# Optimization experiments

Measured on AMD Instinct MI355X. Metric: run time of the kernel, lower is better.

Reference implementation:

```python
import jax, jax.numpy as jnp
import numpy as np

# YOLOLayer config (matches init_kwargs)
ANCHORS = [(0.1, 0.13), (0.3, 0.35), (0.6, 0.55)]  # (w, h) as fraction of image
NUM_CLASSES = 80
STRIDE = 8
NA = len(ANCHORS)


def setup_inputs() -> dict:
    key = jax.random.key(0)
    B, C, G = 16, NA * (NUM_CLASSES + 5), 64
    x = jax.random.normal(key, (B, C, G, G), dtype=jnp.float32)
    return {"x": x}


def reference(x):
    B = x.shape[0]
    g0, g1 = x.shape[2], x.shape[3]
    nC = NUM_CLASSES
    # [B, nA, g0, g1, 5+nC]
    pred = x.reshape(B, NA, nC + 5, g0, g1).transpose(0, 1, 3, 4, 2)
    sx = jax.nn.sigmoid(pred[..., 0])
    sy = jax.nn.sigmoid(pred[..., 1])
    w = pred[..., 2]
    h = pred[..., 3]
    pred_conf = jax.nn.sigmoid(pred[..., 4])
    pred_cls = jax.nn.sigmoid(pred[..., 5:])

    # grid offsets: grid_x varies along last dim, grid_y along dim -2 (torch semantics)
    grid_x = jnp.arange(g1, dtype=x.dtype)[None, None, None, :]
    grid_y = jnp.arange(g0, dtype=x.dtype)[None, None, :, None]
    scaled = jnp.asarray([(aw * g0, ah * g1) for aw, ah in ANCHORS], dtype=x.dtype)
    anchor_w = scaled[:, 0].reshape(1, NA, 1, 1)
    anchor_h = scaled[:, 1].reshape(1, NA, 1, 1)

    # torch uses .data (detached) for pred_boxes -> stop_gradient for faithfulness
    pred_boxes = jnp.stack(
        [sx + grid_x, sy + grid_y, jnp.exp(w) * anchor_w, jnp.exp(h) * anchor_h],
        axis=-1,
    )
    pred_boxes = jax.lax.stop_gradient(pred_boxes)

    boxes = pred_boxes.reshape(B, -1, 4) * STRIDE
    conf = pred_conf.reshape(B, -1, 1)
    cls = pred_cls.reshape(B, -1, nC)
    return boxes, conf, cls
```

## Files before the change

kernel.cpp:

```cpp
#include <hip/hip_runtime.h>


#define NB 16
#define NA 3
#define NC 80
#define GG 4096
#define CH 85
#define S  64
#define NG (CH * (S / 4))
#define GPW (NG / 4)
#define NT 4
#define GRID (NB * NA * (GG / S) / NT)

__device__ __forceinline__ float sigmoidf(float v) {
    return 1.0f / (1.0f + __expf(-v));
}

__device__ __forceinline__ int lidx(int ch, int p) {
    int g = (p >> 2) ^ ((ch >> 2) & 7);
    return (ch << 6) + (g << 2) + (p & 3);
}

__global__ __launch_bounds__(256) void yolo_kernel(const float* __restrict__ x,
                                                   float* __restrict__ out) {
    __shared__ float lds[2][CH * S];

    const int tid  = threadIdx.x;
    const int lane = tid & 63;
    const int wv   = tid >> 6;

    float* __restrict__ boxes = out;
    float* __restrict__ conf  = out + (size_t)NB * NA * GG * 4;
    float* __restrict__ cls   = out + (size_t)NB * NA * GG * 5;

    auto stage = [&](int tg, int buf) {
        const float* __restrict__ xin =
            x + (size_t)(tg >> 6) * CH * GG + (tg & 63) * S;
        #pragma unroll
        for (int it = 0; it < 6; ++it) {
            int g0 = wv * GPW + it * 64;
            if (it * 64 + lane < GPW) {
                int g   = g0 + lane;
                int ch  = g >> 4;
                int p4  = g & 15;
                int sp4 = p4 ^ ((ch >> 2) & 7);
                const float* gp = xin + (size_t)ch * GG + (sp4 << 2);
                float* lp = &lds[buf][g0 << 2];
                __builtin_amdgcn_global_load_lds(
                    (const __attribute__((address_space(1))) void*)gp,
                    (__attribute__((address_space(3))) void*)lp,
                    16, 0, 0);
            }
        }
    };

    auto compute = [&](int tg, int buf) {
        const float* __restrict__ L = lds[buf];
        const int ba  = tg >> 6;
        const int a   = ba % NA;
        const int s0  = (tg & 63) * S;
        const int loc = ba * GG + s0;

        const float anchor_w[NA] = {0.1f * 64 * 8, 0.3f * 64 * 8, 0.6f * 64 * 8};
        const float anchor_h[NA] = {0.13f * 64 * 8, 0.35f * 64 * 8, 0.55f * 64 * 8};

        if (tid < S) {
            int p  = tid;
            int sp = s0 + p;
            float gx = (float)(sp & 63);
            float gy = (float)(sp >> 6);
            float4 bx;
            bx.x = (sigmoidf(L[lidx(0, p)]) + gx) * 8.0f;
            bx.y = (sigmoidf(L[lidx(1, p)]) + gy) * 8.0f;
            bx.z = __expf(L[lidx(2, p)]) * anchor_w[a];
            bx.w = __expf(L[lidx(3, p)]) * anchor_h[a];
            reinterpret_cast<float4*>(boxes)[loc + p] = bx;
            conf[loc + p] = sigmoidf(L[lidx(4, p)]);
        }

        float4* __restrict__ cls4 =
            reinterpret_cast<float4*>(cls) + (size_t)loc * 20;
        #pragma unroll
        for (int i0 = 0; i0 < 5; ++i0) {
            int i  = i0 * 256 + tid;
            int p  = i / 20;
            int c4 = i % 20;
            int r  = 5 + (c4 << 2);
            float4 v;
            v.x = sigmoidf(L[lidx(r + 0, p)]);
            v.y = sigmoidf(L[lidx(r + 1, p)]);
            v.z = sigmoidf(L[lidx(r + 2, p)]);
            v.w = sigmoidf(L[lidx(r + 3, p)]);
            cls4[i] = v;
        }
    };

    const int tg0 = blockIdx.x * NT;

    stage(tg0, 0);
    #pragma unroll
    for (int k = 0; k < NT; ++k) {
        if (k + 1 < NT) {
            stage(tg0 + k + 1, (k + 1) & 1);
            asm volatile("s_waitcnt vmcnt(6)" ::: "memory");
        } else {
            asm volatile("s_waitcnt vmcnt(0)" ::: "memory");
        }
        __builtin_amdgcn_s_barrier();
        __builtin_amdgcn_sched_barrier(0);
        compute(tg0 + k, k & 1);
        __builtin_amdgcn_s_barrier();
    }
}

extern "C" void kernel_launch(void* const* d_in, const int* in_sizes, int n_in,
                              void* d_out, int out_size, void* d_ws, size_t ws_size,
                              hipStream_t stream) {
    const float* x = (const float*)d_in[0];
    float* out = (float*)d_out;
    yolo_kernel<<<dim3(GRID), 256, 0, stream>>>(x, out);
}
```

Measured before the change: 25.17 us.

## Spread box work across all waves, use nontemporal stores and remap blocks over XCDs

Box and conf computation now uses all four waves, with each lane producing one box component, instead of leaving one wave to do it. All output stores become nontemporal. Block indices are remapped across the eight XCDs. The staging loop is manually unrolled, with vmcnt waits adjusted so that stores are counted alongside loads. This targets write-bandwidth efficiency and load imbalance, but the hand-tuned vmcnt counts are fragile.

After: 25.18 us. No clear change (+0.0%).

```diff
diff --git a/kernel.cpp b/kernel.cpp
--- a/kernel.cpp
+++ b/kernel.cpp
@@ -9,8 +9,8 @@
 #define S  64
 #define NG (CH * (S / 4))
 #define GPW (NG / 4)
-#define NT 4
-#define GRID (NB * NA * (GG / S) / NT)
+
+typedef float f32x4 __attribute__((ext_vector_type(4)));
 
 __device__ __forceinline__ float sigmoidf(float v) {
     return 1.0f / (1.0f + __expf(-v));
@@ -29,9 +29,12 @@
     const int lane = tid & 63;
     const int wv   = tid >> 6;
 
-    float* __restrict__ boxes = out;
-    float* __restrict__ conf  = out + (size_t)NB * NA * GG * 4;
-    float* __restrict__ cls   = out + (size_t)NB * NA * GG * 5;
+    const int wg  = (blockIdx.x & 7) * 96 + (blockIdx.x >> 3);
+    const int tg0 = wg * 4;
+
+    float* __restrict__ boxesF = out;
+    float* __restrict__ conf   = out + (size_t)NB * NA * GG * 4;
+    f32x4* __restrict__ cls4   = (f32x4*)(out + (size_t)NB * NA * GG * 5);
 
     auto stage = [&](int tg, int buf) {
         const float* __restrict__ xin =
@@ -58,59 +61,71 @@
         const float* __restrict__ L = lds[buf];
         const int ba  = tg >> 6;
         const int a   = ba % NA;
-        const int s0  = (tg & 63) * S;
-        const int loc = ba * GG + s0;
+        const int row = tg & 63;
+        const int loc = ba * GG + row * S;
 
-        const float anchor_w[NA] = {0.1f * 64 * 8, 0.3f * 64 * 8, 0.6f * 64 * 8};
-        const float anchor_h[NA] = {0.13f * 64 * 8, 0.35f * 64 * 8, 0.55f * 64 * 8};
+        const float aw = (a == 0) ? 0.1f * 64 * 8
+                       : (a == 1) ? 0.3f * 64 * 8 : 0.6f * 64 * 8;
+        const float ah = (a == 0) ? 0.13f * 64 * 8
+                       : (a == 1) ? 0.35f * 64 * 8 : 0.55f * 64 * 8;
 
-        if (tid < S) {
-            int p  = tid;
-            int sp = s0 + p;
-            float gx = (float)(sp & 63);
-            float gy = (float)(sp >> 6);
-            float4 bx;
-            bx.x = (sigmoidf(L[lidx(0, p)]) + gx) * 8.0f;
-            bx.y = (sigmoidf(L[lidx(1, p)]) + gy) * 8.0f;
-            bx.z = __expf(L[lidx(2, p)]) * anchor_w[a];
-            bx.w = __expf(L[lidx(3, p)]) * anchor_h[a];
-            reinterpret_cast<float4*>(boxes)[loc + p] = bx;
-            conf[loc + p] = sigmoidf(L[lidx(4, p)]);
+        {
+            int p    = wv * 16 + (lane >> 2);
+            int comp = lane & 3;
+            float v  = L[lidx(comp, p)];
+            float e  = __expf(comp >= 2 ? v : -v);
+            float sg = 1.0f / (1.0f + e);
+            float gxy  = (comp == 0) ? (float)p : (float)row;
+            float anch = (comp == 2) ? aw : ah;
+            float r = (comp < 2) ? (sg + gxy) * 8.0f : e * anch;
+            __builtin_nontemporal_store(
+                r, &boxesF[((size_t)loc + wv * 16) * 4 + lane]);
+            if (lane < 16) {
+                float cv = sigmoidf(L[lidx(4, wv * 16 + lane)]);
+                __builtin_nontemporal_store(cv, &conf[loc + wv * 16 + lane]);
+            }
         }
 
-        float4* __restrict__ cls4 =
-            reinterpret_cast<float4*>(cls) + (size_t)loc * 20;
         #pragma unroll
         for (int i0 = 0; i0 < 5; ++i0) {
             int i  = i0 * 256 + tid;
             int p  = i / 20;
-            int c4 = i % 20;
-            int r  = 5 + (c4 << 2);
-            float4 v;
-            v.x = sigmoidf(L[lidx(r + 0, p)]);
-            v.y = sigmoidf(L[lidx(r + 1, p)]);
-            v.z = sigmoidf(L[lidx(r + 2, p)]);
-            v.w = sigmoidf(L[lidx(r + 3, p)]);
-            cls4[i] = v;
+            int c4 = i - p * 20;
+            int r0 = 5 + (c4 << 2);
+            f32x4 v;
+            v.x = sigmoidf(L[lidx(r0 + 0, p)]);
+            v.y = sigmoidf(L[lidx(r0 + 1, p)]);
+            v.z = sigmoidf(L[lidx(r0 + 2, p)]);
+            v.w = sigmoidf(L[lidx(r0 + 3, p)]);
+            __builtin_nontemporal_store(v, &cls4[(size_t)loc * 20 + i]);
         }
     };
 
-    const int tg0 = blockIdx.x * NT;
+    stage(tg0 + 0, 0);
+    stage(tg0 + 1, 1);
+    asm volatile("s_waitcnt vmcnt(6)" ::: "memory");
+    __builtin_amdgcn_s_barrier();
+    __builtin_amdgcn_sched_barrier(0);
+    compute(tg0 + 0, 0);
+    __builtin_amdgcn_s_barrier();
 
-    stage(tg0, 0);
-    #pragma unroll
-    for (int k = 0; k < NT; ++k) {
-        if (k + 1 < NT) {
-            stage(tg0 + k + 1, (k + 1) & 1);
-            asm volatile("s_waitcnt vmcnt(6)" ::: "memory");
-        } else {
-            asm volatile("s_waitcnt vmcnt(0)" ::: "memory");
-        }
-        __builtin_amdgcn_s_barrier();
-        __builtin_amdgcn_sched_barrier(0);
-        compute(tg0 + k, k & 1);
-        __builtin_amdgcn_s_barrier();
-    }
+    stage(tg0 + 2, 0);
+    asm volatile("s_waitcnt vmcnt(13)" ::: "memory");
+    __builtin_amdgcn_s_barrier();
+    __builtin_amdgcn_sched_barrier(0);
+    compute(tg0 + 1, 1);
+    __builtin_amdgcn_s_barrier();
+
+    stage(tg0 + 3, 1);
+    asm volatile("s_waitcnt vmcnt(13)" ::: "memory");
+    __builtin_amdgcn_s_barrier();
+    __builtin_amdgcn_sched_barrier(0);
+    compute(tg0 + 2, 0);
+
+    asm volatile("s_waitcnt vmcnt(7)" ::: "memory");
+    __builtin_amdgcn_s_barrier();
+    __builtin_amdgcn_sched_barrier(0);
+    compute(tg0 + 3, 1);
 }
 
 extern "C" void kernel_launch(void* const* d_in, const int* in_sizes, int n_in,
@@ -118,5 +133,5 @@
                               hipStream_t stream) {
     const float* x = (const float*)d_in[0];
     float* out = (float*)d_out;
-    yolo_kernel<<<dim3(GRID), 256, 0, stream>>>(x, out);
+    yolo_kernel<<<dim3(768), 256, 0, stream>>>(x, out);
 }
```
